# Kernel tuning notes

Hardware: AMD Instinct MI355X
Metric: run time of the kernel (lower is better)

The kernel has to match this reference:

```python
import jax, jax.numpy as jnp
import numpy as np

C = 512
NUM_HEADS = 8
HEAD_DIM = C // NUM_HEADS


def setup_inputs() -> dict:
    key = jax.random.key(0)
    ks = jax.random.split(key, 5)
    B, H, W = 4, 48, 48
    x = jax.random.normal(ks[0], (B, C, H, W), dtype=jnp.float32)
    # 1x1 conv weights == dense matrices over channel dim
    Wqkv = jax.random.normal(ks[1], (3 * C, C), dtype=jnp.float32) * (1.0 / np.sqrt(C))
    bqkv = jax.random.normal(ks[2], (3 * C,), dtype=jnp.float32) * 0.01
    Wout = jax.random.normal(ks[3], (C, C), dtype=jnp.float32) * (1.0 / np.sqrt(C))
    bout = jax.random.normal(ks[4], (C,), dtype=jnp.float32) * 0.01
    return {"x": x, "Wqkv": Wqkv, "bqkv": bqkv, "Wout": Wout, "bout": bout}


def reference(x, Wqkv, bqkv, Wout, bout):
    B, Cc, H, W = x.shape
    S = H * W
    # qkv 1x1 conv: [B, 3C, H, W] -> reshape (B, 3, heads, head_dim, S)
    qkv = jnp.einsum('bchw,oc->bohw', x, Wqkv) + bqkv[None, :, None, None]
    qkv = qkv.reshape(B, 3, NUM_HEADS, HEAD_DIM, S)
    q, k, v = qkv[:, 0], qkv[:, 1], qkv[:, 2]  # [B, h, d, S]
    # tokens along S: q^T k, scaled softmax
    scale = HEAD_DIM ** -0.5
    attn = jnp.einsum('bhds,bhdt->bhst', q, k) * scale  # [B, h, S, S]
    attn = jax.nn.softmax(attn, axis=-1)
    out = jnp.einsum('bhst,bhdt->bhds', attn, v)  # [B, h, d, S]
    out = out.reshape(B, Cc, H, W)
    out = jnp.einsum('bchw,oc->bohw', out, Wout) + bout[None, :, None, None]
    return out
```

## Files before the change

kernel.cpp:

```cpp
#include <hip/hip_runtime.h>

#define S_LEN 2304
#define CDIM  512
#define NHEAD 8

typedef __attribute__((ext_vector_type(4))) float f32x4;
typedef __attribute__((ext_vector_type(8))) _Float16 f16x8;
typedef __attribute__((ext_vector_type(2))) __fp16 fp16x2r;
typedef _Float16 h16;

#define QSCALE 0.18033688011112042f

__device__ __forceinline__ float fexp2(float x) {
#if __has_builtin(__builtin_amdgcn_exp2f)
    return __builtin_amdgcn_exp2f(x);
#else
    return exp2f(x);
#endif
}

__device__ __forceinline__ void gll16(const h16* g, h16* l) {
    __builtin_amdgcn_global_load_lds(
        (const __attribute__((address_space(1))) unsigned int*)g,
        (__attribute__((address_space(3))) unsigned int*)l, 16, 0, 0);
}

__global__ __launch_bounds__(256) void xpose_x(
    const float* __restrict__ x, h16* __restrict__ xT)
{
    const int s0 = blockIdx.x * 64;
    const int c0 = blockIdx.y * 64;
    const int b  = blockIdx.z;
    __shared__ h16 Ts[64][76];

    const int t  = threadIdx.x;
    const int cq = t >> 4;
    const int sq = t & 15;

    const float* xb = x + ((size_t)b * CDIM + c0 + cq * 4) * S_LEN + s0 + sq * 4;
    float4 r0 = *(const float4*)(xb);
    float4 r1 = *(const float4*)(xb + S_LEN);
    float4 r2 = *(const float4*)(xb + 2 * S_LEN);
    float4 r3 = *(const float4*)(xb + 3 * S_LEN);

    union { h16 h[4]; uint2 u; } pk;
    pk.h[0]=(h16)r0.x; pk.h[1]=(h16)r1.x; pk.h[2]=(h16)r2.x; pk.h[3]=(h16)r3.x;
    *(uint2*)&Ts[sq*4+0][cq*4] = pk.u;
    pk.h[0]=(h16)r0.y; pk.h[1]=(h16)r1.y; pk.h[2]=(h16)r2.y; pk.h[3]=(h16)r3.y;
    *(uint2*)&Ts[sq*4+1][cq*4] = pk.u;
    pk.h[0]=(h16)r0.z; pk.h[1]=(h16)r1.z; pk.h[2]=(h16)r2.z; pk.h[3]=(h16)r3.z;
    *(uint2*)&Ts[sq*4+2][cq*4] = pk.u;
    pk.h[0]=(h16)r0.w; pk.h[1]=(h16)r1.w; pk.h[2]=(h16)r2.w; pk.h[3]=(h16)r3.w;
    *(uint2*)&Ts[sq*4+3][cq*4] = pk.u;

    __syncthreads();
    const int s  = t >> 2;
    const int cc = (t & 3) * 16;
    uint2 a0 = *(uint2*)&Ts[s][cc + 0];
    uint2 a1 = *(uint2*)&Ts[s][cc + 4];
    uint2 a2 = *(uint2*)&Ts[s][cc + 8];
    uint2 a3 = *(uint2*)&Ts[s][cc + 12];
    h16* dst = xT + ((size_t)b * S_LEN + s0 + s) * CDIM + c0 + cc;
    uint4 w0 = make_uint4(a0.x, a0.y, a1.x, a1.y);
    uint4 w1 = make_uint4(a2.x, a2.y, a3.x, a3.y);
    *(uint4*)dst       = w0;
    *(uint4*)(dst + 8) = w1;
}

__global__ __launch_bounds__(256) void wconv(
    const float* __restrict__ Wq, const float* __restrict__ Wo,
    h16* __restrict__ Wq_h, h16* __restrict__ Wo_h)
{
    const int NQ = 1536 * 512;
    const int NO = 512 * 512;
    int i = (blockIdx.x * 256 + threadIdx.x) * 4;
    if (i >= NQ + NO) return;
    float4 v;
    h16* dst;
    if (i < NQ) { v = *(const float4*)(Wq + i);        dst = Wq_h + i; }
    else        { v = *(const float4*)(Wo + (i - NQ)); dst = Wo_h + (i - NQ); }
    union { h16 h[4]; uint2 u; } pk;
    pk.h[0]=(h16)v.x; pk.h[1]=(h16)v.y; pk.h[2]=(h16)v.z; pk.h[3]=(h16)v.w;
    *(uint2*)dst = pk.u;
}

__global__ __launch_bounds__(256) void gemm_qkv(
    const h16* __restrict__ Wh, const float* __restrict__ bqkv,
    const h16* __restrict__ xT, h16* __restrict__ qT, h16* __restrict__ kT,
    h16* __restrict__ vN)
{
    const int n0 = blockIdx.x * 128;
    const int m0 = blockIdx.y * 128;
    const int b  = blockIdx.z;
    __shared__ h16 Ws[128 * 64];
    __shared__ h16 Xs[128 * 64];

    const int tid = threadIdx.x;
    const int lid = tid & 63, w = tid >> 6;
    const int g = lid >> 4, ln = lid & 15;
    const int wm = w & 1, wn = w >> 1;
    const int srow = lid >> 3;
    const int sblk = (lid & 7) ^ (srow & 7);

    f32x4 acc[4][4];
#pragma unroll
    for (int i = 0; i < 4; i++)
#pragma unroll
        for (int j = 0; j < 4; j++) acc[i][j] = (f32x4)0.f;

    const h16* Wbase = Wh + (size_t)m0 * CDIM;
    const h16* Xbase = xT + ((size_t)b * S_LEN + n0) * CDIM;
    const bool vblk = (m0 >= 1024);

    for (int kt = 0; kt < CDIM; kt += 64) {
        __syncthreads();
#pragma unroll
        for (int i = 0; i < 4; i++) {
            const int row0 = w * 32 + i * 8;
            gll16(Wbase + (size_t)(row0 + srow) * CDIM + kt + sblk * 8, &Ws[row0 * 64]);
            gll16(Xbase + (size_t)(row0 + srow) * CDIM + kt + sblk * 8, &Xs[row0 * 64]);
        }
        __syncthreads();

#pragma unroll
        for (int kc = 0; kc < 2; kc++) {
            f16x8 af[4], bf[4];
#pragma unroll
            for (int i = 0; i < 4; i++) {
                const int ra = wm * 64 + i * 16 + ln;
                const int ca = (kc * 64 + g * 16) ^ ((ra & 7) << 4);
                af[i] = *(const f16x8*)&Ws[ra * 64 + ca / 2];
                const int rb = wn * 64 + i * 16 + ln;
                const int cb = (kc * 64 + g * 16) ^ ((rb & 7) << 4);
                bf[i] = *(const f16x8*)&Xs[rb * 64 + cb / 2];
            }
            if (!vblk) {
#pragma unroll
                for (int i = 0; i < 4; i++)
#pragma unroll
                    for (int j = 0; j < 4; j++)
                        acc[i][j] = __builtin_amdgcn_mfma_f32_16x16x32_f16(
                            af[i], bf[j], acc[i][j], 0, 0, 0);
            } else {
#pragma unroll
                for (int i = 0; i < 4; i++)
#pragma unroll
                    for (int j = 0; j < 4; j++)
                        acc[i][j] = __builtin_amdgcn_mfma_f32_16x16x32_f16(
                            bf[i], af[j], acc[i][j], 0, 0, 0);
            }
        }
    }

    if (!vblk) {
#pragma unroll
        for (int i = 0; i < 4; i++) {
            const int mb = m0 + wm * 64 + i * 16 + 4 * g;
            const float4 bv = *(const float4*)&bqkv[mb];
            const int mloc = mb & 511;
            const int hh = mloc >> 6, d0 = mloc & 63;
            const bool isq = (mb < 512);
            const float scl = isq ? QSCALE : 1.0f;
            h16* base = (isq ? qT : kT);
#pragma unroll
            for (int j = 0; j < 4; j++) {
                const int n = n0 + wn * 64 + j * 16 + ln;
                union { h16 h[4]; uint2 u; } pk;
                pk.h[0] = (h16)((acc[i][j][0] + bv.x) * scl);
                pk.h[1] = (h16)((acc[i][j][1] + bv.y) * scl);
                pk.h[2] = (h16)((acc[i][j][2] + bv.z) * scl);
                pk.h[3] = (h16)((acc[i][j][3] + bv.w) * scl);
                *(uint2*)(base + (((size_t)b * 8 + hh) * S_LEN + n) * 64 + d0) = pk.u;
            }
        }
    } else {
#pragma unroll
        for (int j = 0; j < 4; j++) {
            const int m = m0 + wm * 64 + j * 16 + ln;
            const float bias = bqkv[m];
            const int mloc = m - 1024;
            const int hh = mloc >> 6, d = mloc & 63;
            h16* base = vN + (((size_t)b * 8 + hh) * 64 + d) * S_LEN;
#pragma unroll
            for (int i = 0; i < 4; i++) {
                const int nb = n0 + wn * 64 + i * 16 + 4 * g;
                union { h16 h[4]; uint2 u; } pk;
                pk.h[0] = (h16)(acc[i][j][0] + bias);
                pk.h[1] = (h16)(acc[i][j][1] + bias);
                pk.h[2] = (h16)(acc[i][j][2] + bias);
                pk.h[3] = (h16)(acc[i][j][3] + bias);
                *(uint2*)(base + nb) = pk.u;
            }
        }
    }
}

__global__ __launch_bounds__(384, 4) void attn_f16(
    const h16* __restrict__ qT, const h16* __restrict__ kT,
    const h16* __restrict__ vN, h16* __restrict__ attT)
{
    const int s0 = blockIdx.x * 96;
    const int h  = blockIdx.y;
    const int b  = blockIdx.z;
    __shared__ h16 Ks[2][64 * 64];
    __shared__ h16 Vs[2][64 * 64];
    __shared__ h16 Ps[96 * 64];

    const int tid = threadIdx.x;
    const int lid = tid & 63, w = tid >> 6;
    const int g = lid >> 4, ln = lid & 15;
    const int srow = lid >> 3;
    const int sblk = (lid & 7) ^ (srow & 7);

    const h16* qb = qT + ((size_t)b * 8 + h) * S_LEN * 64;
    const h16* kb = kT + ((size_t)b * 8 + h) * S_LEN * 64;
    const h16* vb = vN + ((size_t)b * 8 + h) * 64 * S_LEN;

    f16x8 qreg[2];
    {
        const h16* qrow = qb + (size_t)(s0 + 16 * w + ln) * 64;
        qreg[0] = *(const f16x8*)(qrow + g * 8);
        qreg[1] = *(const f16x8*)(qrow + 32 + g * 8);
    }

    for (int c = w; c < 16; c += 6) {
        if (c < 8)
            gll16(kb + (size_t)(c * 8 + srow) * 64 + sblk * 8, &Ks[0][c * 8 * 64]);
        else
            gll16(vb + (size_t)((c - 8) * 8 + srow) * S_LEN + sblk * 8,
                  &Vs[0][(c - 8) * 8 * 64]);
    }
    __syncthreads();

    f16x8 ones;
#pragma unroll
    for (int i = 0; i < 8; i++) ones[i] = (h16)1.0f;

    float m_run = -1e30f;
    f32x4 oacc[4], lacc;
#pragma unroll
    for (int i = 0; i < 4; i++) oacc[i] = (f32x4)0.f;
    lacc = (f32x4)0.f;

    int cur = 0;
    for (int kt = 0; kt < S_LEN; kt += 64, cur ^= 1) {
        if (kt + 64 < S_LEN) {
            for (int c = w; c < 16; c += 6) {
                if (c < 8)
                    gll16(kb + (size_t)(kt + 64 + c * 8 + srow) * 64 + sblk * 8,
                          &Ks[cur ^ 1][c * 8 * 64]);
                else
                    gll16(vb + (size_t)((c - 8) * 8 + srow) * S_LEN + kt + 64 + sblk * 8,
                          &Vs[cur ^ 1][(c - 8) * 8 * 64]);
            }
        }
        const h16* Kc = Ks[cur];
        const h16* Vc = Vs[cur];

        f32x4 sacc[4];
#pragma unroll
        for (int tb = 0; tb < 4; tb++) sacc[tb] = (f32x4)0.f;
#pragma unroll
        for (int c = 0; c < 2; c++) {
#pragma unroll
            for (int tb = 0; tb < 4; tb++) {
                const int row = tb * 16 + ln;
                const int cb = (c * 64 + g * 16) ^ ((row & 7) << 4);
                f16x8 kf = *(const f16x8*)&Kc[row * 64 + cb / 2];
                sacc[tb] = __builtin_amdgcn_mfma_f32_16x16x32_f16(kf, qreg[c], sacc[tb], 0, 0, 0);
            }
        }

        float m0 = fmaxf(fmaxf(sacc[0][0], sacc[0][1]), fmaxf(sacc[0][2], sacc[0][3]));
        float m1 = fmaxf(fmaxf(sacc[1][0], sacc[1][1]), fmaxf(sacc[1][2], sacc[1][3]));
        float m2 = fmaxf(fmaxf(sacc[2][0], sacc[2][1]), fmaxf(sacc[2][2], sacc[2][3]));
        float m3 = fmaxf(fmaxf(sacc[3][0], sacc[3][1]), fmaxf(sacc[3][2], sacc[3][3]));
        float mloc = fmaxf(fmaxf(m0, m1), fmaxf(m2, m3));
        mloc = fmaxf(mloc, __shfl_xor(mloc, 16));
        mloc = fmaxf(mloc, __shfl_xor(mloc, 32));

        if (!__all(mloc <= m_run + 8.0f)) {
            const float mnew = fmaxf(m_run, mloc);
            const float resc = fexp2(m_run - mnew);
#pragma unroll
            for (int db = 0; db < 4; db++)
#pragma unroll
                for (int r = 0; r < 4; r++) oacc[db][r] *= resc;
#pragma unroll
            for (int r = 0; r < 4; r++) lacc[r] *= resc;
            m_run = mnew;
        }

#pragma unroll
        for (int tb = 0; tb < 4; tb++) {
            union { fp16x2r v[2]; uint2 u; } pk;
            pk.v[0] = __builtin_amdgcn_cvt_pkrtz(fexp2(sacc[tb][0] - m_run),
                                                 fexp2(sacc[tb][1] - m_run));
            pk.v[1] = __builtin_amdgcn_cvt_pkrtz(fexp2(sacc[tb][2] - m_run),
                                                 fexp2(sacc[tb][3] - m_run));
            const int cb = (tb * 32 + g * 8) ^ ((ln & 7) << 4);
            *(uint2*)&Ps[(16 * w + ln) * 64 + cb / 2] = pk.u;
        }

#pragma unroll
        for (int c = 0; c < 2; c++) {
            const int cp = (c * 64 + g * 16) ^ ((ln & 7) << 4);
            f16x8 pf = *(const f16x8*)&Ps[(16 * w + ln) * 64 + cp / 2];
            lacc = __builtin_amdgcn_mfma_f32_16x16x32_f16(ones, pf, lacc, 0, 0, 0);
#pragma unroll
            for (int db = 0; db < 4; db++) {
                const int row = db * 16 + ln;
                const int cb = (c * 64 + g * 16) ^ ((row & 7) << 4);
                f16x8 vf = *(const f16x8*)&Vc[row * 64 + cb / 2];
                oacc[db] = __builtin_amdgcn_mfma_f32_16x16x32_f16(vf, pf, oacc[db], 0, 0, 0);
            }
        }
        __syncthreads();
    }

    const float inv = 1.0f / lacc[0];
    h16* ob = attT + ((size_t)b * S_LEN + s0 + 16 * w + ln) * CDIM + h * 64;
#pragma unroll
    for (int db = 0; db < 4; db++) {
        union { h16 h[4]; uint2 u; } pk;
#pragma unroll
        for (int r = 0; r < 4; r++) pk.h[r] = (h16)(oacc[db][r] * inv);
        *(uint2*)(ob + db * 16 + 4 * g) = pk.u;
    }
}

__global__ __launch_bounds__(256) void gemm_out(
    const h16* __restrict__ attT, const h16* __restrict__ Wh,
    const float* __restrict__ bout, float* __restrict__ out)
{
    const int n0 = blockIdx.x * 128;
    const int m0 = blockIdx.y * 128;
    const int b  = blockIdx.z;
    __shared__ h16 Ws[128 * 64];
    __shared__ h16 Xs[128 * 64];

    const int tid = threadIdx.x;
    const int lid = tid & 63, w = tid >> 6;
    const int g = lid >> 4, ln = lid & 15;
    const int wm = w & 1, wn = w >> 1;
    const int srow = lid >> 3;
    const int sblk = (lid & 7) ^ (srow & 7);

    f32x4 acc[4][4];
#pragma unroll
    for (int i = 0; i < 4; i++)
#pragma unroll
        for (int j = 0; j < 4; j++) acc[i][j] = (f32x4)0.f;

    const h16* Wbase = Wh + (size_t)m0 * CDIM;
    const h16* Xbase = attT + ((size_t)b * S_LEN + n0) * CDIM;

    for (int kt = 0; kt < CDIM; kt += 64) {
        __syncthreads();
#pragma unroll
        for (int i = 0; i < 4; i++) {
            const int row0 = w * 32 + i * 8;
            gll16(Wbase + (size_t)(row0 + srow) * CDIM + kt + sblk * 8, &Ws[row0 * 64]);
            gll16(Xbase + (size_t)(row0 + srow) * CDIM + kt + sblk * 8, &Xs[row0 * 64]);
        }
        __syncthreads();

#pragma unroll
        for (int kc = 0; kc < 2; kc++) {
            f16x8 af[4], bf[4];
#pragma unroll
            for (int i = 0; i < 4; i++) {
                const int ra = wm * 64 + i * 16 + ln;
                const int ca = (kc * 64 + g * 16) ^ ((ra & 7) << 4);
                af[i] = *(const f16x8*)&Ws[ra * 64 + ca / 2];
                const int rb = wn * 64 + i * 16 + ln;
                const int cb = (kc * 64 + g * 16) ^ ((rb & 7) << 4);
                bf[i] = *(const f16x8*)&Xs[rb * 64 + cb / 2];
            }
#pragma unroll
            for (int i = 0; i < 4; i++)
#pragma unroll
                for (int j = 0; j < 4; j++)
                    acc[i][j] = __builtin_amdgcn_mfma_f32_16x16x32_f16(
                        bf[i], af[j], acc[i][j], 0, 0, 0);
        }
    }

#pragma unroll
    for (int j = 0; j < 4; j++) {
        const int m = m0 + wm * 64 + j * 16 + ln;
        const float bias = bout[m];
        float* base = out + ((size_t)b * CDIM + m) * S_LEN;
#pragma unroll
        for (int i = 0; i < 4; i++) {
            const int nb = n0 + wn * 64 + i * 16 + 4 * g;
            float4 o;
            o.x = acc[i][j][0] + bias;
            o.y = acc[i][j][1] + bias;
            o.z = acc[i][j][2] + bias;
            o.w = acc[i][j][3] + bias;
            *(float4*)(base + nb) = o;
        }
    }
}

extern "C" void kernel_launch(void* const* d_in, const int* in_sizes, int n_in,
                              void* d_out, int out_size, void* d_ws, size_t ws_size,
                              hipStream_t stream)
{
    const float* x    = (const float*)d_in[0];
    const float* Wqkv = (const float*)d_in[1];
    const float* bqkv = (const float*)d_in[2];
    const float* Wout = (const float*)d_in[3];
    const float* bout = (const float*)d_in[4];
    float* out = (float*)d_out;

    h16* xT   = (h16*)d_ws;
    h16* Wq_h = xT   + (size_t)4 * S_LEN * CDIM;
    h16* Wo_h = Wq_h + (size_t)1536 * 512;
    h16* qT   = Wo_h + (size_t)512 * 512;
    h16* kT   = qT   + (size_t)4 * 8 * S_LEN * 64;
    h16* vN   = kT   + (size_t)4 * 8 * S_LEN * 64;
    h16* attT = vN   + (size_t)4 * 8 * S_LEN * 64;

    xpose_x <<<dim3(36, 8, 4),  256, 0, stream>>>(x, xT);
    wconv   <<<1024,            256, 0, stream>>>(Wqkv, Wout, Wq_h, Wo_h);
    gemm_qkv<<<dim3(18, 12, 4), 256, 0, stream>>>(Wq_h, bqkv, xT, qT, kT, vN);
    attn_f16<<<dim3(24, 8, 4),  384, 0, stream>>>(qT, kT, vN, attT);
    gemm_out<<<dim3(18, 4, 4),  256, 0, stream>>>(attT, Wo_h, bout, out);
}
```

Measured before the change: 155.4 us.

## Switch attention to 32x32 MFMA with register-resident P via permlane32 swap

Rewrites the attention kernel to use 32x32x16 MFMA tiles, with each wave owning 32 query rows (128 per block, 4 waves). The softmax probabilities stay in registers and are rearranged with v_permlane32_swap instead of going through an LDS P buffer. The row sum is computed with scalar adds instead of a ones-matrix MFMA. This removes LDS round-trips and the extra MFMA for the sum, but the grid shrinks to 576 blocks and per-thread register pressure rises.

New measurement: 136.5 us. -12.2%, faster.

```diff
diff --git a/kernel.cpp b/kernel.cpp
--- a/kernel.cpp
+++ b/kernel.cpp
@@ -4,9 +4,10 @@
 #define CDIM  512
 #define NHEAD 8
 
-typedef __attribute__((ext_vector_type(4))) float f32x4;
-typedef __attribute__((ext_vector_type(8))) _Float16 f16x8;
-typedef __attribute__((ext_vector_type(2))) __fp16 fp16x2r;
+typedef __attribute__((ext_vector_type(4)))  float f32x4;
+typedef __attribute__((ext_vector_type(16))) float f32x16;
+typedef __attribute__((ext_vector_type(8)))  _Float16 f16x8;
+typedef __attribute__((ext_vector_type(2)))  __fp16 fp16x2r;
 typedef _Float16 h16;
 
 #define QSCALE 0.18033688011112042f
@@ -17,6 +18,12 @@
 #else
     return exp2f(x);
 #endif
+}
+
+__device__ __forceinline__ unsigned cvtpk(float a, float b) {
+    union { fp16x2r v; unsigned u; } c;
+    c.v = __builtin_amdgcn_cvt_pkrtz(a, b);
+    return c.u;
 }
 
 __device__ __forceinline__ void gll16(const h16* g, h16* l) {
@@ -195,20 +202,19 @@
     }
 }
 
-__global__ __launch_bounds__(384, 4) void attn_f16(
+__global__ __launch_bounds__(256, 4) void attn_f16(
     const h16* __restrict__ qT, const h16* __restrict__ kT,
     const h16* __restrict__ vN, h16* __restrict__ attT)
 {
-    const int s0 = blockIdx.x * 96;
+    const int s0 = blockIdx.x * 128;
     const int h  = blockIdx.y;
     const int b  = blockIdx.z;
     __shared__ h16 Ks[2][64 * 64];
     __shared__ h16 Vs[2][64 * 64];
-    __shared__ h16 Ps[96 * 64];
 
     const int tid = threadIdx.x;
     const int lid = tid & 63, w = tid >> 6;
-    const int g = lid >> 4, ln = lid & 15;
+    const int l31 = lid & 31, hi = lid >> 5;
     const int srow = lid >> 3;
     const int sblk = (lid & 7) ^ (srow & 7);
 
@@ -216,14 +222,17 @@
     const h16* kb = kT + ((size_t)b * 8 + h) * S_LEN * 64;
     const h16* vb = vN + ((size_t)b * 8 + h) * 64 * S_LEN;
 
-    f16x8 qreg[2];
+    const int sq = s0 + w * 32 + l31;
+
+    f16x8 qf[4];
     {
-        const h16* qrow = qb + (size_t)(s0 + 16 * w + ln) * 64;
-        qreg[0] = *(const f16x8*)(qrow + g * 8);
-        qreg[1] = *(const f16x8*)(qrow + 32 + g * 8);
-    }
-
-    for (int c = w; c < 16; c += 6) {
+        const h16* qrow = qb + (size_t)sq * 64;
+#pragma unroll
+        for (int ds = 0; ds < 4; ds++)
+            qf[ds] = *(const f16x8*)(qrow + ds * 16 + hi * 8);
+    }
+
+    for (int c = w; c < 16; c += 4) {
         if (c < 8)
             gll16(kb + (size_t)(c * 8 + srow) * 64 + sblk * 8, &Ks[0][c * 8 * 64]);
         else
@@ -232,20 +241,13 @@
     }
     __syncthreads();
 
-    f16x8 ones;
-#pragma unroll
-    for (int i = 0; i < 8; i++) ones[i] = (h16)1.0f;
-
-    float m_run = -1e30f;
-    f32x4 oacc[4], lacc;
-#pragma unroll
-    for (int i = 0; i < 4; i++) oacc[i] = (f32x4)0.f;
-    lacc = (f32x4)0.f;
+    float m_run = -1e30f, l_run = 0.f;
+    f32x16 oacc0 = (f32x16)0.f, oacc1 = (f32x16)0.f;
 
     int cur = 0;
     for (int kt = 0; kt < S_LEN; kt += 64, cur ^= 1) {
         if (kt + 64 < S_LEN) {
-            for (int c = w; c < 16; c += 6) {
+            for (int c = w; c < 16; c += 4) {
                 if (c < 8)
                     gll16(kb + (size_t)(kt + 64 + c * 8 + srow) * 64 + sblk * 8,
                           &Ks[cur ^ 1][c * 8 * 64]);
@@ -257,75 +259,98 @@
         const h16* Kc = Ks[cur];
         const h16* Vc = Vs[cur];
 
-        f32x4 sacc[4];
-#pragma unroll
-        for (int tb = 0; tb < 4; tb++) sacc[tb] = (f32x4)0.f;
-#pragma unroll
-        for (int c = 0; c < 2; c++) {
-#pragma unroll
-            for (int tb = 0; tb < 4; tb++) {
-                const int row = tb * 16 + ln;
-                const int cb = (c * 64 + g * 16) ^ ((row & 7) << 4);
-                f16x8 kf = *(const f16x8*)&Kc[row * 64 + cb / 2];
-                sacc[tb] = __builtin_amdgcn_mfma_f32_16x16x32_f16(kf, qreg[c], sacc[tb], 0, 0, 0);
-            }
-        }
-
-        float m0 = fmaxf(fmaxf(sacc[0][0], sacc[0][1]), fmaxf(sacc[0][2], sacc[0][3]));
-        float m1 = fmaxf(fmaxf(sacc[1][0], sacc[1][1]), fmaxf(sacc[1][2], sacc[1][3]));
-        float m2 = fmaxf(fmaxf(sacc[2][0], sacc[2][1]), fmaxf(sacc[2][2], sacc[2][3]));
-        float m3 = fmaxf(fmaxf(sacc[3][0], sacc[3][1]), fmaxf(sacc[3][2], sacc[3][3]));
-        float mloc = fmaxf(fmaxf(m0, m1), fmaxf(m2, m3));
-        mloc = fmaxf(mloc, __shfl_xor(mloc, 16));
+        f32x16 sacc0 = (f32x16)0.f, sacc1 = (f32x16)0.f;
+#pragma unroll
+        for (int ds = 0; ds < 4; ds++) {
+            const int bc = 2 * ds + hi;
+            {
+                const int row = l31;
+                f16x8 kf = *(const f16x8*)&Kc[row * 64 + ((bc ^ (row & 7)) * 8)];
+                sacc0 = __builtin_amdgcn_mfma_f32_32x32x16_f16(kf, qf[ds], sacc0, 0, 0, 0);
+            }
+            {
+                const int row = 32 + l31;
+                f16x8 kf = *(const f16x8*)&Kc[row * 64 + ((bc ^ (row & 7)) * 8)];
+                sacc1 = __builtin_amdgcn_mfma_f32_32x32x16_f16(kf, qf[ds], sacc1, 0, 0, 0);
+            }
+        }
+
+        float mloc = -1e30f;
+#pragma unroll
+        for (int r = 0; r < 16; r++) {
+            mloc = fmaxf(mloc, sacc0[r]);
+            mloc = fmaxf(mloc, sacc1[r]);
+        }
         mloc = fmaxf(mloc, __shfl_xor(mloc, 32));
 
         if (!__all(mloc <= m_run + 8.0f)) {
             const float mnew = fmaxf(m_run, mloc);
             const float resc = fexp2(m_run - mnew);
 #pragma unroll
-            for (int db = 0; db < 4; db++)
-#pragma unroll
-                for (int r = 0; r < 4; r++) oacc[db][r] *= resc;
-#pragma unroll
-            for (int r = 0; r < 4; r++) lacc[r] *= resc;
+            for (int r = 0; r < 16; r++) { oacc0[r] *= resc; oacc1[r] *= resc; }
+            l_run *= resc;
             m_run = mnew;
         }
 
-#pragma unroll
-        for (int tb = 0; tb < 4; tb++) {
-            union { fp16x2r v[2]; uint2 u; } pk;
-            pk.v[0] = __builtin_amdgcn_cvt_pkrtz(fexp2(sacc[tb][0] - m_run),
-                                                 fexp2(sacc[tb][1] - m_run));
-            pk.v[1] = __builtin_amdgcn_cvt_pkrtz(fexp2(sacc[tb][2] - m_run),
-                                                 fexp2(sacc[tb][3] - m_run));
-            const int cb = (tb * 32 + g * 8) ^ ((ln & 7) << 4);
-            *(uint2*)&Ps[(16 * w + ln) * 64 + cb / 2] = pk.u;
-        }
-
-#pragma unroll
-        for (int c = 0; c < 2; c++) {
-            const int cp = (c * 64 + g * 16) ^ ((ln & 7) << 4);
-            f16x8 pf = *(const f16x8*)&Ps[(16 * w + ln) * 64 + cp / 2];
-            lacc = __builtin_amdgcn_mfma_f32_16x16x32_f16(ones, pf, lacc, 0, 0, 0);
-#pragma unroll
-            for (int db = 0; db < 4; db++) {
-                const int row = db * 16 + ln;
-                const int cb = (c * 64 + g * 16) ^ ((row & 7) << 4);
-                f16x8 vf = *(const f16x8*)&Vc[row * 64 + cb / 2];
-                oacc[db] = __builtin_amdgcn_mfma_f32_16x16x32_f16(vf, pf, oacc[db], 0, 0, 0);
+        float lsum = 0.f;
+#pragma unroll
+        for (int r = 0; r < 16; r++) {
+            sacc0[r] = fexp2(sacc0[r] - m_run); lsum += sacc0[r];
+        }
+#pragma unroll
+        for (int r = 0; r < 16; r++) {
+            sacc1[r] = fexp2(sacc1[r] - m_run); lsum += sacc1[r];
+        }
+        l_run += lsum + __shfl_xor(lsum, 32);
+
+        f16x8 pf[4];
+#pragma unroll
+        for (int i = 0; i < 4; i++) {
+            const int bse = (i & 1) * 8;
+            float pv[8];
+#pragma unroll
+            for (int r = 0; r < 8; r++)
+                pv[r] = (i < 2) ? sacc0[bse + r] : sacc1[bse + r];
+            unsigned X0 = cvtpk(pv[0], pv[1]);
+            unsigned X1 = cvtpk(pv[2], pv[3]);
+            unsigned Y0 = cvtpk(pv[4], pv[5]);
+            unsigned Y1 = cvtpk(pv[6], pv[7]);
+            asm("v_permlane32_swap_b32 %0, %1" : "+v"(X0), "+v"(Y0));
+            asm("v_permlane32_swap_b32 %0, %1" : "+v"(X1), "+v"(Y1));
+            union { unsigned u[4]; f16x8 v; } pkk;
+            pkk.u[0] = X0; pkk.u[1] = X1; pkk.u[2] = Y0; pkk.u[3] = Y1;
+            pf[i] = pkk.v;
+        }
+
+#pragma unroll
+        for (int i = 0; i < 4; i++) {
+            const int bc = 2 * i + hi;
+            {
+                const int row = l31;
+                f16x8 vf = *(const f16x8*)&Vc[row * 64 + ((bc ^ (row & 7)) * 8)];
+                oacc0 = __builtin_amdgcn_mfma_f32_32x32x16_f16(vf, pf[i], oacc0, 0, 0, 0);
+            }
+            {
+                const int row = 32 + l31;
+                f16x8 vf = *(const f16x8*)&Vc[row * 64 + ((bc ^ (row & 7)) * 8)];
+                oacc1 = __builtin_amdgcn_mfma_f32_32x32x16_f16(vf, pf[i], oacc1, 0, 0, 0);
             }
         }
         __syncthreads();
     }
 
-    const float inv = 1.0f / lacc[0];
-    h16* ob = attT + ((size_t)b * S_LEN + s0 + 16 * w + ln) * CDIM + h * 64;
-#pragma unroll
-    for (int db = 0; db < 4; db++) {
-        union { h16 h[4]; uint2 u; } pk;
-#pragma unroll
-        for (int r = 0; r < 4; r++) pk.h[r] = (h16)(oacc[db][r] * inv);
-        *(uint2*)(ob + db * 16 + 4 * g) = pk.u;
+    const float inv = 1.0f / l_run;
+    h16* ob = attT + ((size_t)b * S_LEN + sq) * CDIM + h * 64;
+#pragma unroll
+    for (int gi = 0; gi < 4; gi++) {
+        union { h16 hh[4]; uint2 u; } p0, p1;
+#pragma unroll
+        for (int r = 0; r < 4; r++) {
+            p0.hh[r] = (h16)(oacc0[gi * 4 + r] * inv);
+            p1.hh[r] = (h16)(oacc1[gi * 4 + r] * inv);
+        }
+        *(uint2*)(ob + 8 * gi + 4 * hi)      = p0.u;
+        *(uint2*)(ob + 32 + 8 * gi + 4 * hi) = p1.u;
     }
 }
 
@@ -426,6 +451,6 @@
     xpose_x <<<dim3(36, 8, 4),  256, 0, stream>>>(x, xT);
     wconv   <<<1024,            256, 0, stream>>>(Wqkv, Wout, Wq_h, Wo_h);
     gemm_qkv<<<dim3(18, 12, 4), 256, 0, stream>>>(Wq_h, bqkv, xT, qT, kT, vN);
-    attn_f16<<<dim3(24, 8, 4),  384, 0, stream>>>(qT, kT, vN, attT);
+    attn_f16<<<dim3(18, 8, 4),  256, 0, stream>>>(qT, kT, vN, attT);
     gemm_out<<<dim3(18, 4, 4),  256, 0, stream>>>(attT, Wo_h, bout, out);
 }
```
